# Optimization experiments

Hardware: AMD Instinct MI355X
Metric: run time of the kernel (lower is better)

Reference implementation:

```python
import jax, jax.numpy as jnp
import numpy as np

N_NODES = 50000
HEADS1 = 4
NEG_SLOPE = 0.2
EPS = 1e-16


def gat_conv(x, edge_index, W, att_src, att_dst, bias, heads, out_ch, concat):
    # edge_index: [2, E] with self-loops already appended by caller
    src, dst = edge_index[0], edge_index[1]
    N = x.shape[0]
    h = (x @ W).reshape(N, heads, out_ch)                      # [N, H, C]
    a_src = jnp.sum(h * att_src, axis=-1)                      # [N, H]
    a_dst = jnp.sum(h * att_dst, axis=-1)                      # [N, H]
    e = a_src[src] + a_dst[dst]                                # [E, H]
    e = jnp.where(e > 0, e, NEG_SLOPE * e)                     # leaky_relu
    m = jax.ops.segment_max(e, dst, num_segments=N)            # [N, H]
    alpha = jnp.exp(e - m[dst])                                # [E, H]
    denom = jax.ops.segment_sum(alpha, dst, num_segments=N)    # [N, H]
    alpha = alpha / (denom[dst] + EPS)                         # [E, H]
    msg = alpha[:, :, None] * h[src]                           # [E, H, C]
    out = jax.ops.segment_sum(msg, dst, num_segments=N)        # [N, H, C]
    if concat:
        out = out.reshape(N, heads * out_ch)
    else:
        out = out.mean(axis=1)
    return out + bias, alpha


def setup_inputs() -> dict:
    key = jax.random.key(0)
    ks = jax.random.split(key, 12)
    N, F, H, heads, C, E = N_NODES, 256, 64, HEADS1, 40, 800000
    g = 0.1
    return {
        "x": jax.random.normal(ks[0], (N, F), dtype=jnp.float32),
        "edge_index": jax.random.randint(ks[1], (2, E), 0, N, dtype=jnp.int32),
        "W1": jax.random.normal(ks[2], (F, heads * H), dtype=jnp.float32) * g,
        "att_src1": jax.random.normal(ks[3], (heads, H), dtype=jnp.float32) * g,
        "att_dst1": jax.random.normal(ks[4], (heads, H), dtype=jnp.float32) * g,
        "b1": jnp.zeros((heads * H,), dtype=jnp.float32),
        "W2": jax.random.normal(ks[5], (heads * H, C), dtype=jnp.float32) * g,
        "att_src2": jax.random.normal(ks[6], (1, C), dtype=jnp.float32) * g,
        "att_dst2": jax.random.normal(ks[7], (1, C), dtype=jnp.float32) * g,
        "b2": jnp.zeros((C,), dtype=jnp.float32),
    }


def reference(x, edge_index, W1, att_src1, att_dst1, b1, W2, att_src2, att_dst2, b2):
    N = x.shape[0]
    # add self-loops (PyG GATConv default)
    loops = jnp.arange(N, dtype=edge_index.dtype)
    ei = jnp.concatenate([edge_index, jnp.stack([loops, loops])], axis=1)
    # dropout is identity in eval mode
    h1, alpha = gat_conv(x, ei, W1, att_src1, att_dst1, b1,
                         HEADS1, W1.shape[1] // HEADS1, concat=True)
    h1 = jax.nn.elu(h1)
    h2, _ = gat_conv(h1, ei, W2, att_src2, att_dst2, b2,
                     1, W2.shape[1], concat=False)
    return jax.nn.log_softmax(h2, axis=1), alpha
```

## Files before the change

kernel.cpp:

```cpp
#include <hip/hip_runtime.h>
#include <math.h>

#define N_NODES 50000
#define HC1 256
#define H1 4
#define C2 40
#define C2P 64
#define E0 800000
#define ET 850000
#define NEG_SLOPE 0.2f
#define EPS_A 1e-16f

typedef __bf16 bf16x8 __attribute__((ext_vector_type(8)));
typedef float f32x4 __attribute__((ext_vector_type(4)));
typedef unsigned short u16x8 __attribute__((ext_vector_type(8)));


__device__ inline unsigned short f2bf(float f) {
    unsigned u = __float_as_uint(f);
    return (unsigned short)((u + 0x7FFFu + ((u >> 16) & 1u)) >> 16);
}
__device__ inline float bf2f(unsigned short h) { return __uint_as_float(((unsigned)h) << 16); }
__device__ inline float bf_lo(unsigned q) { return __uint_as_float(q << 16); }
__device__ inline float bf_hi(unsigned q) { return __uint_as_float(q & 0xFFFF0000u); }


__global__ void fill_int_kernel(int* __restrict__ p, int n, int v) {
    int i = blockIdx.x * blockDim.x + threadIdx.x;
    if (i < n) p[i] = v;
}

__device__ inline int edge_src(const int* __restrict__ ei, int e) {
    return (e < E0) ? ei[e] : (e - E0);
}
__device__ inline int edge_dst(const int* __restrict__ ei, int e) {
    return (e < E0) ? ei[E0 + e] : (e - E0);
}


__global__ void f32_to_bf16_kernel(const float* __restrict__ src,
                                   unsigned short* __restrict__ dst, int n4) {
    int i = blockIdx.x * blockDim.x + threadIdx.x;
    if (i >= n4) return;
    float4 v = ((const float4*)src)[i];
    ushort4 w;
    w.x = f2bf(v.x); w.y = f2bf(v.y); w.z = f2bf(v.z); w.w = f2bf(v.w);
    ((ushort4*)dst)[i] = w;
}

__global__ void w1_transpose_kernel(const float* __restrict__ W1,
                                    unsigned short* __restrict__ Wt) {
    int tid = blockIdx.x * blockDim.x + threadIdx.x;
    if (tid >= 256 * 256) return;
    int n = tid >> 8, k = tid & 255;
    Wt[tid] = f2bf(W1[k * 256 + n]);
}

__global__ void w2_transpose_pad_kernel(const float* __restrict__ W2,
                                        unsigned short* __restrict__ Wt) {
    int tid = blockIdx.x * blockDim.x + threadIdx.x;
    if (tid >= 64 * 256) return;
    int n = tid >> 8, k = tid & 255;
    Wt[tid] = (n < C2) ? f2bf(W2[k * C2 + n]) : (unsigned short)0;
}


__global__ void hist_kernel(const int* __restrict__ ei, int* __restrict__ deg) {
    int e = blockIdx.x * blockDim.x + threadIdx.x;
    if (e >= ET) return;
    atomicAdd(&deg[edge_dst(ei, e)], 1);
}

__global__ __launch_bounds__(256) void scan_block_kernel(const int* __restrict__ deg,
                                                         int* __restrict__ excl,
                                                         int* __restrict__ bsum) {
    __shared__ int tmp[256];
    int t = threadIdx.x;
    int i = blockIdx.x * 256 + t;
    int v = (i < N_NODES) ? deg[i] : 0;
    tmp[t] = v;
    __syncthreads();
#pragma unroll
    for (int o = 1; o < 256; o <<= 1) {
        int x = (t >= o) ? tmp[t - o] : 0;
        __syncthreads();
        tmp[t] += x;
        __syncthreads();
    }
    if (i < N_NODES) excl[i] = tmp[t] - v;
    if (t == 255) bsum[blockIdx.x] = tmp[255];
}

#define NSCAN_B 196

__global__ __launch_bounds__(256) void scan_top_kernel(int* __restrict__ bsum) {
    __shared__ int tmp[256];
    int t = threadIdx.x;
    int v = (t < NSCAN_B) ? bsum[t] : 0;
    tmp[t] = v;
    __syncthreads();
#pragma unroll
    for (int o = 1; o < 256; o <<= 1) {
        int x = (t >= o) ? tmp[t - o] : 0;
        __syncthreads();
        tmp[t] += x;
        __syncthreads();
    }
    if (t < NSCAN_B) bsum[t] = tmp[t] - v;
}

__global__ __launch_bounds__(256) void scan_add_kernel(int* __restrict__ offsets,
                                                       int* __restrict__ cursor,
                                                       const int* __restrict__ bsum) {
    int i = blockIdx.x * 256 + threadIdx.x;
    if (i < N_NODES) {
        int v = offsets[i] + bsum[blockIdx.x];
        offsets[i] = v;
        cursor[i] = v;
    }
    if (i == 0) offsets[N_NODES] = ET;
}

__global__ void scatter_kernel(const int* __restrict__ ei, int* __restrict__ cursor,
                               int2* __restrict__ csr_es) {
    int e = blockIdx.x * blockDim.x + threadIdx.x;
    if (e >= ET) return;
    int d = edge_dst(ei, e);
    int pos = atomicAdd(&cursor[d], 1);
    csr_es[pos] = make_int2(e, edge_src(ei, e));
}


template <int TBM, int TBN, int WROWS, int WCOLS>
__global__ __launch_bounds__(256) void gemm_mfma_kernel(const unsigned short* __restrict__ Abf,
                                                        const unsigned short* __restrict__ Bt,
                                                        unsigned short* __restrict__ Cbf,
                                                        const float* __restrict__ att_s,
                                                        const float* __restrict__ att_d,
                                                        float* __restrict__ a_src_o,
                                                        float* __restrict__ a_dst_o,
                                                        int M, int Nc, int attN, int hstride) {
    static_assert(TBM == WROWS * 64 && TBN == WCOLS * 64, "tile");
    constexpr int LDK = 40;
    __shared__ alignas(16) unsigned short As[TBM * LDK];
    __shared__ alignas(16) unsigned short Bs[TBN * LDK];
    const int t = threadIdx.x;
    const int lane = t & 63;
    const int w = t >> 6;
    const int quad = lane >> 4;
    const int l16 = lane & 15;
    const int wm = (w / WCOLS) * 64;
    const int wn = (w % WCOLS) * 64;
    const int bm = blockIdx.x * TBM;
    const int bn = blockIdx.y * TBN;

    f32x4 acc[4][4] = {};

    for (int k0 = 0; k0 < 256; k0 += 32) {
        __syncthreads();
#pragma unroll
        for (int i = 0; i < TBM / 64; ++i) {
            int idx = t + i * 256;
            int row = idx >> 2, seg = idx & 3;
            u16x8 v = {};
            if (bm + row < M)
                v = *(const u16x8*)(Abf + (size_t)(bm + row) * 256 + k0 + seg * 8);
            *(u16x8*)&As[row * LDK + seg * 8] = v;
        }
#pragma unroll
        for (int i = 0; i < TBN / 64; ++i) {
            int idx = t + i * 256;
            int row = idx >> 2, seg = idx & 3;
            u16x8 v = *(const u16x8*)(Bt + (size_t)(bn + row) * 256 + k0 + seg * 8);
            *(u16x8*)&Bs[row * LDK + seg * 8] = v;
        }
        __syncthreads();

        bf16x8 af[4], bfr[4];
#pragma unroll
        for (int mi = 0; mi < 4; ++mi)
            af[mi] = *(const bf16x8*)&As[(wm + mi * 16 + l16) * LDK + quad * 8];
#pragma unroll
        for (int ni = 0; ni < 4; ++ni)
            bfr[ni] = *(const bf16x8*)&Bs[(wn + ni * 16 + l16) * LDK + quad * 8];
#pragma unroll
        for (int mi = 0; mi < 4; ++mi)
#pragma unroll
            for (int ni = 0; ni < 4; ++ni)
                acc[mi][ni] = __builtin_amdgcn_mfma_f32_16x16x32_bf16(
                    af[mi], bfr[ni], acc[mi][ni], 0, 0, 0);
    }

#pragma unroll
    for (int mi = 0; mi < 4; ++mi)
#pragma unroll
        for (int ni = 0; ni < 4; ++ni)
#pragma unroll
            for (int r = 0; r < 4; ++r) {
                int row = bm + wm + mi * 16 + quad * 4 + r;
                int col = bn + wn + ni * 16 + l16;
                if (row < M)
                    Cbf[(size_t)row * Nc + col] = f2bf(acc[mi][ni][r]);
            }

    float asc[4], adc[4];
#pragma unroll
    for (int ni = 0; ni < 4; ++ni) {
        int col = bn + wn + ni * 16 + l16;
        bool valid = col < attN;
        asc[ni] = valid ? att_s[col] : 0.f;
        adc[ni] = valid ? att_d[col] : 0.f;
    }
    float vs[16], vd[16];
#pragma unroll
    for (int mi = 0; mi < 4; ++mi)
#pragma unroll
        for (int r = 0; r < 4; ++r) {
            float s = 0.f, dd = 0.f;
#pragma unroll
            for (int ni = 0; ni < 4; ++ni) {
                s += acc[mi][ni][r] * asc[ni];
                dd += acc[mi][ni][r] * adc[ni];
            }
            vs[mi * 4 + r] = s;
            vd[mi * 4 + r] = dd;
        }
#pragma unroll
    for (int k = 0; k < 4; ++k) {
        const int o = 1 << k;
        const int b = (l16 >> k) & 1;
#pragma unroll
        for (int j = 0; j < (8 >> k); ++j) {
            float lo = vs[2 * j], hi = vs[2 * j + 1];
            float keep = b ? hi : lo, send = b ? lo : hi;
            vs[j] = keep + __shfl_xor(send, o);
            lo = vd[2 * j]; hi = vd[2 * j + 1];
            keep = b ? hi : lo; send = b ? lo : hi;
            vd[j] = keep + __shfl_xor(send, o);
        }
    }
    {
        int mi = l16 >> 2, r = l16 & 3;
        int row = bm + wm + mi * 16 + quad * 4 + r;
        int head = (bn + wn) >> 6;
        if (row < M) {
            a_src_o[(size_t)row * hstride + head] = vs[0];
            a_dst_o[(size_t)row * hstride + head] = vd[0];
        }
    }
}


#define DCAP 512
__global__ __launch_bounds__(256) void l1_fused_kernel(const int* __restrict__ off,
                                                       const int2* __restrict__ csr_es,
                                                       const float* __restrict__ a_src,
                                                       const float* __restrict__ a_dst,
                                                       const unsigned* __restrict__ h1bf,
                                                       const float* __restrict__ b1,
                                                       float* __restrict__ alpha_out,
                                                       unsigned* __restrict__ out1bf) {
    __shared__ int   s_src[DCAP];
    __shared__ int   s_eid[DCAP];
    __shared__ float s_al[H1][DCAP];
    __shared__ float s_stat[H1][2];
    __shared__ float s_comb[2][128][2];
    int d = blockIdx.x;
    int t = threadIdx.x;
    int hd = t >> 6, lane = t & 63;
    int beg = off[d], end = off[d + 1];
    int deg = end - beg;
    float ad = a_dst[d * H1 + hd];

    float elc[8];
    float mx = -INFINITY;
    int c = 0;
    for (int idx = beg + lane; idx < end; idx += 64, ++c) {
        int2 es = csr_es[idx];
        int j = idx - beg;
        if (hd == 0 && j < DCAP) { s_src[j] = es.y; s_eid[j] = es.x; }
        float el = a_src[es.y * H1 + hd] + ad;
        el = el > 0.f ? el : NEG_SLOPE * el;
        if (c < 8) elc[c] = el;
        mx = fmaxf(mx, el);
    }
#pragma unroll
    for (int o = 32; o; o >>= 1) mx = fmaxf(mx, __shfl_xor(mx, o));

    float sum = 0.f;
    c = 0;
    for (int idx = beg + lane; idx < end; idx += 64, ++c) {
        float el;
        if (c < 8) el = elc[c];
        else {
            int2 es = csr_es[idx];
            el = a_src[es.y * H1 + hd] + ad;
            el = el > 0.f ? el : NEG_SLOPE * el;
        }
        float p = __expf(el - mx);
        int j = idx - beg;
        if (j < DCAP) s_al[hd][j] = p;
        sum += p;
    }
#pragma unroll
    for (int o = 32; o; o >>= 1) sum += __shfl_xor(sum, o);
    float inv = 1.f / (sum + EPS_A);
    if (lane == 0) { s_stat[hd][0] = mx; s_stat[hd][1] = inv; }
    __syncthreads();

    int n = min(deg, DCAP);
    {
        float i0 = s_stat[0][1], i1 = s_stat[1][1], i2 = s_stat[2][1], i3 = s_stat[3][1];
        for (int j = t; j < n; j += 256) {
            float4 a4 = make_float4(s_al[0][j] * i0, s_al[1][j] * i1,
                                    s_al[2][j] * i2, s_al[3][j] * i3);
            *(float4*)&alpha_out[(size_t)s_eid[j] * H1] = a4;
        }
    }
    for (int idx = beg + DCAP + lane; idx < end; idx += 64) {
        int2 es = csr_es[idx];
        float el = a_src[es.y * H1 + hd] + ad;
        el = el > 0.f ? el : NEG_SLOPE * el;
        alpha_out[(size_t)es.x * H1 + hd] = __expf(el - mx) * inv;
    }

    int tt = t & 127, eo = t >> 7, head = tt >> 5;
    float acc0 = 0.f, acc1 = 0.f;
    int j = eo;
    for (; j + 6 < n; j += 8) {
        int s0 = s_src[j], s1 = s_src[j + 2], s2 = s_src[j + 4], s3 = s_src[j + 6];
        float a0 = s_al[head][j], a1 = s_al[head][j + 2];
        float a2 = s_al[head][j + 4], a3 = s_al[head][j + 6];
        unsigned q0 = h1bf[(size_t)s0 * 128 + tt];
        unsigned q1 = h1bf[(size_t)s1 * 128 + tt];
        unsigned q2 = h1bf[(size_t)s2 * 128 + tt];
        unsigned q3 = h1bf[(size_t)s3 * 128 + tt];
        acc0 += a0 * bf_lo(q0) + a1 * bf_lo(q1) + a2 * bf_lo(q2) + a3 * bf_lo(q3);
        acc1 += a0 * bf_hi(q0) + a1 * bf_hi(q1) + a2 * bf_hi(q2) + a3 * bf_hi(q3);
    }
    for (; j < n; j += 2) {
        unsigned q = h1bf[(size_t)s_src[j] * 128 + tt];
        float a = s_al[head][j];
        acc0 += a * bf_lo(q);
        acc1 += a * bf_hi(q);
    }
    for (int jj = DCAP + eo; jj < deg; jj += 2) {
        int2 es = csr_es[beg + jj];
        float el = a_src[es.y * H1 + head] + a_dst[d * H1 + head];
        el = el > 0.f ? el : NEG_SLOPE * el;
        float p = __expf(el - s_stat[head][0]);
        unsigned q = h1bf[(size_t)es.y * 128 + tt];
        acc0 += p * bf_lo(q);
        acc1 += p * bf_hi(q);
    }
    s_comb[eo][tt][0] = acc0;
    s_comb[eo][tt][1] = acc1;
    __syncthreads();
    if (t < 128) {
        float invh = s_stat[t >> 5][1];
        float2 bb = *(const float2*)&b1[2 * t];
        float v0 = (s_comb[0][t][0] + s_comb[1][t][0]) * invh + bb.x;
        float v1 = (s_comb[0][t][1] + s_comb[1][t][1]) * invh + bb.y;
        v0 = v0 > 0.f ? v0 : __expf(v0) - 1.f;
        v1 = v1 > 0.f ? v1 : __expf(v1) - 1.f;
        out1bf[(size_t)d * 128 + t] = ((unsigned)f2bf(v1) << 16) | (unsigned)f2bf(v0);
    }
}


__global__ __launch_bounds__(256) void l2_fused_kernel(const int* __restrict__ off,
                                                       const int2* __restrict__ csr_es,
                                                       const float* __restrict__ a_src,
                                                       const float* __restrict__ a_dst,
                                                       const unsigned* __restrict__ h2bf,
                                                       const float* __restrict__ b2,
                                                       float* __restrict__ out) {
    int t = threadIdx.x;
    int lane = t & 63;
    int d = blockIdx.x * 4 + (t >> 6);
    if (d >= N_NODES) return;
    int beg = off[d], end = off[d + 1];
    int deg = end - beg;
    float ad = a_dst[d];
    int nch = (deg + 63) >> 6;

    float elc[4]; int sc[4];
    float mx = -INFINITY;
    for (int cc = 0; cc < nch; ++cc) {
        int idx = beg + cc * 64 + lane;
        float el = -INFINITY; int s = 0;
        if (idx < end) {
            int2 es = csr_es[idx];
            s = es.y;
            el = a_src[s] + ad;
            el = el > 0.f ? el : NEG_SLOPE * el;
        }
        if (cc < 4) { elc[cc] = el; sc[cc] = s; }
        mx = fmaxf(mx, el);
    }
#pragma unroll
    for (int o = 32; o; o >>= 1) mx = fmaxf(mx, __shfl_xor(mx, o));

    float sum = 0.f;
    for (int cc = 0; cc < nch; ++cc) {
        float p;
        if (cc < 4) {
            p = __expf(elc[cc] - mx);
            elc[cc] = p;
        } else {
            int idx = beg + cc * 64 + lane;
            float el = -INFINITY;
            if (idx < end) {
                int2 es = csr_es[idx];
                el = a_src[es.y] + ad;
                el = el > 0.f ? el : NEG_SLOPE * el;
            }
            p = __expf(el - mx);
        }
        sum += p;
    }
#pragma unroll
    for (int o = 32; o; o >>= 1) sum += __shfl_xor(sum, o);
    float inv = 1.f / (sum + EPS_A);

    int half = lane >> 5, li = lane & 31;
    float acc0 = 0.f, acc1 = 0.f;
    for (int cc = 0; cc < nch; ++cc) {
        int cnt = min(64, deg - cc * 64);
        int my_s; float my_a;
        if (cc < 4) {
            my_s = sc[cc];
            my_a = elc[cc];
        } else {
            int idx = beg + cc * 64 + lane;
            my_s = 0; my_a = 0.f;
            if (idx < end) {
                int2 es = csr_es[idx];
                my_s = es.y;
                float el = a_src[es.y] + ad;
                el = el > 0.f ? el : NEG_SLOPE * el;
                my_a = __expf(el - mx);
            }
        }
        for (int j = 0; j < cnt; j += 2) {
            int jj = j + half;
            int s = __shfl(my_s, jj);
            float a = __shfl(my_a, jj);
            if (jj < cnt) {
                unsigned q = h2bf[(size_t)s * 32 + li];
                acc0 += a * bf_lo(q);
                acc1 += a * bf_hi(q);
            }
        }
    }
    acc0 += __shfl_xor(acc0, 32);
    acc1 += __shfl_xor(acc1, 32);
    acc0 *= inv;
    acc1 *= inv;
    bool act = li < 20;
    float v0 = act ? acc0 + b2[2 * li]     : -INFINITY;
    float v1 = act ? acc1 + b2[2 * li + 1] : -INFINITY;
    float mmx = fmaxf(v0, v1);
#pragma unroll
    for (int o = 16; o; o >>= 1) mmx = fmaxf(mmx, __shfl_xor(mmx, o));
    float ex = act ? __expf(v0 - mmx) + __expf(v1 - mmx) : 0.f;
#pragma unroll
    for (int o = 16; o; o >>= 1) ex += __shfl_xor(ex, o);
    float ls = __logf(ex);
    if (act && half == 0)
        *(float2*)&out[(size_t)d * C2 + 2 * li] = make_float2(v0 - mmx - ls, v1 - mmx - ls);
}


extern "C" void kernel_launch(void* const* d_in, const int* in_sizes, int n_in,
                              void* d_out, int out_size, void* d_ws, size_t ws_size,
                              hipStream_t stream) {
    const float* x   = (const float*)d_in[0];
    const int*   ei  = (const int*)d_in[1];
    const float* W1  = (const float*)d_in[2];
    const float* as1 = (const float*)d_in[3];
    const float* ad1 = (const float*)d_in[4];
    const float* b1  = (const float*)d_in[5];
    const float* W2  = (const float*)d_in[6];
    const float* as2 = (const float*)d_in[7];
    const float* ad2 = (const float*)d_in[8];
    const float* b2  = (const float*)d_in[9];

    float* out   = (float*)d_out;
    float* alpha = out + (size_t)N_NODES * C2;

    unsigned* u32    = (unsigned*)d_ws;
    unsigned* h1bf   = u32;
    unsigned* xbf    = h1bf + 6400000;
    unsigned* h2bf   = xbf + 6400000;
    unsigned* w1t    = h2bf + 1600000;
    unsigned* w2t    = w1t + 32768;
    float* a_src1    = (float*)(w2t + 8192);
    float* a_dst1    = a_src1 + 200000;
    float* a_src2    = a_dst1 + 200000;
    float* a_dst2    = a_src2 + 50000;
    int*   deg       = (int*)(a_dst2 + 50000);
    int*   offs      = deg + 50000;
    int*   cursor    = offs + 50001;
    int*   bsum      = cursor + 50000;
    int2*  csr_es    = (int2*)(bsum + 257);
    unsigned* out1bf = xbf;

    const int TB = 256;
    const int EB = (ET + TB - 1) / TB;

    fill_int_kernel<<<(N_NODES + TB - 1) / TB, TB, 0, stream>>>(deg, N_NODES, 0);
    hist_kernel<<<EB, TB, 0, stream>>>(ei, deg);
    scan_block_kernel<<<NSCAN_B, TB, 0, stream>>>(deg, offs, bsum);
    scan_top_kernel<<<1, TB, 0, stream>>>(bsum);
    scan_add_kernel<<<NSCAN_B, TB, 0, stream>>>(offs, cursor, bsum);
    scatter_kernel<<<EB, TB, 0, stream>>>(ei, cursor, csr_es);

    f32_to_bf16_kernel<<<(3200000 + TB - 1) / TB, TB, 0, stream>>>(
        x, (unsigned short*)xbf, 3200000);
    w1_transpose_kernel<<<(65536 + TB - 1) / TB, TB, 0, stream>>>(W1, (unsigned short*)w1t);
    w2_transpose_pad_kernel<<<(16384 + TB - 1) / TB, TB, 0, stream>>>(W2, (unsigned short*)w2t);

    gemm_mfma_kernel<128, 128, 2, 2><<<dim3((N_NODES + 127) / 128, 2), TB, 0, stream>>>(
        (const unsigned short*)xbf, (const unsigned short*)w1t, (unsigned short*)h1bf,
        as1, ad1, a_src1, a_dst1, N_NODES, HC1, 256, H1);
    l1_fused_kernel<<<N_NODES, TB, 0, stream>>>(offs, csr_es, a_src1, a_dst1,
                                                h1bf, b1, alpha, out1bf);

    gemm_mfma_kernel<256, 64, 4, 1><<<dim3((N_NODES + 255) / 256, 1), TB, 0, stream>>>(
        (const unsigned short*)out1bf, (const unsigned short*)w2t, (unsigned short*)h2bf,
        as2, ad2, a_src2, a_dst2, N_NODES, C2P, C2, 1);
    l2_fused_kernel<<<(N_NODES + 3) / 4, TB, 0, stream>>>(offs, csr_es, a_src2, a_dst2,
                                                          h2bf, b2, out);
}
```

Before: 414.2 us.

## Map one wavefront per node in layer-1 GAT aggregation and merge conversion kernels

The layer-1 fused kernel moves from one 256-thread block per destination node to one 64-lane wavefront per node, four nodes per block. Each lane handles all four heads with float4 loads of a_src, a_dst and alpha, and gathers h1 rows with 64-bit loads. The first 64 edges are staged in shared memory, and longer adjacency lists are walked chunk by chunk with shuffle broadcasts. The three input conversion and transpose kernels become one launch, and the softmax shuffle reductions in both layers stop after covering only the active degree. This targets the idle threads and block overhead that come with low average degree, at the cost of less parallelism on high-degree nodes.

Result: faster. 382.0 us (-7.8%).

```diff
diff --git a/kernel.cpp b/kernel.cpp
--- a/kernel.cpp
+++ b/kernel.cpp
@@ -20,7 +20,6 @@
     unsigned u = __float_as_uint(f);
     return (unsigned short)((u + 0x7FFFu + ((u >> 16) & 1u)) >> 16);
 }
-__device__ inline float bf2f(unsigned short h) { return __uint_as_float(((unsigned)h) << 16); }
 __device__ inline float bf_lo(unsigned q) { return __uint_as_float(q << 16); }
 __device__ inline float bf_hi(unsigned q) { return __uint_as_float(q & 0xFFFF0000u); }
 
@@ -38,30 +37,31 @@
 }
 
 
-__global__ void f32_to_bf16_kernel(const float* __restrict__ src,
-                                   unsigned short* __restrict__ dst, int n4) {
-    int i = blockIdx.x * blockDim.x + threadIdx.x;
-    if (i >= n4) return;
-    float4 v = ((const float4*)src)[i];
-    ushort4 w;
-    w.x = f2bf(v.x); w.y = f2bf(v.y); w.z = f2bf(v.z); w.w = f2bf(v.w);
-    ((ushort4*)dst)[i] = w;
-}
-
-__global__ void w1_transpose_kernel(const float* __restrict__ W1,
-                                    unsigned short* __restrict__ Wt) {
+#define CV_X 3200000
+#define CV_W1 65536
+#define CV_W2 16384
+
+__global__ void convert_all_kernel(const float* __restrict__ x,
+                                   const float* __restrict__ W1,
+                                   const float* __restrict__ W2,
+                                   ushort4* __restrict__ xbf,
+                                   unsigned short* __restrict__ w1t,
+                                   unsigned short* __restrict__ w2t) {
     int tid = blockIdx.x * blockDim.x + threadIdx.x;
-    if (tid >= 256 * 256) return;
-    int n = tid >> 8, k = tid & 255;
-    Wt[tid] = f2bf(W1[k * 256 + n]);
-}
-
-__global__ void w2_transpose_pad_kernel(const float* __restrict__ W2,
-                                        unsigned short* __restrict__ Wt) {
-    int tid = blockIdx.x * blockDim.x + threadIdx.x;
-    if (tid >= 64 * 256) return;
-    int n = tid >> 8, k = tid & 255;
-    Wt[tid] = (n < C2) ? f2bf(W2[k * C2 + n]) : (unsigned short)0;
+    if (tid < CV_X) {
+        float4 v = ((const float4*)x)[tid];
+        ushort4 w;
+        w.x = f2bf(v.x); w.y = f2bf(v.y); w.z = f2bf(v.z); w.w = f2bf(v.w);
+        xbf[tid] = w;
+    } else if (tid < CV_X + CV_W1) {
+        int i = tid - CV_X;
+        int n = i >> 8, k = i & 255;
+        w1t[i] = f2bf(W1[k * 256 + n]);
+    } else if (tid < CV_X + CV_W1 + CV_W2) {
+        int i = tid - CV_X - CV_W1;
+        int n = i >> 8, k = i & 255;
+        w2t[i] = (n < C2) ? f2bf(W2[k * C2 + n]) : (unsigned short)0;
+    }
 }
 
 
@@ -251,120 +251,164 @@
 }
 
 
-#define DCAP 512
 __global__ __launch_bounds__(256) void l1_fused_kernel(const int* __restrict__ off,
                                                        const int2* __restrict__ csr_es,
-                                                       const float* __restrict__ a_src,
-                                                       const float* __restrict__ a_dst,
+                                                       const float4* __restrict__ a_src4,
+                                                       const float4* __restrict__ a_dst4,
                                                        const unsigned* __restrict__ h1bf,
                                                        const float* __restrict__ b1,
-                                                       float* __restrict__ alpha_out,
+                                                       float4* __restrict__ alpha_out4,
                                                        unsigned* __restrict__ out1bf) {
-    __shared__ int   s_src[DCAP];
-    __shared__ int   s_eid[DCAP];
-    __shared__ float s_al[H1][DCAP];
-    __shared__ float s_stat[H1][2];
-    __shared__ float s_comb[2][128][2];
-    int d = blockIdx.x;
+    __shared__ int    s_w[4][64];
+    __shared__ float4 a_w[4][64];
     int t = threadIdx.x;
-    int hd = t >> 6, lane = t & 63;
+    int w = t >> 6, lane = t & 63;
+    int d = blockIdx.x * 4 + w;
     int beg = off[d], end = off[d + 1];
     int deg = end - beg;
-    float ad = a_dst[d * H1 + hd];
-
-    float elc[8];
-    float mx = -INFINITY;
-    int c = 0;
-    for (int idx = beg + lane; idx < end; idx += 64, ++c) {
-        int2 es = csr_es[idx];
-        int j = idx - beg;
-        if (hd == 0 && j < DCAP) { s_src[j] = es.y; s_eid[j] = es.x; }
-        float el = a_src[es.y * H1 + hd] + ad;
-        el = el > 0.f ? el : NEG_SLOPE * el;
-        if (c < 8) elc[c] = el;
-        mx = fmaxf(mx, el);
-    }
-#pragma unroll
-    for (int o = 32; o; o >>= 1) mx = fmaxf(mx, __shfl_xor(mx, o));
-
-    float sum = 0.f;
-    c = 0;
-    for (int idx = beg + lane; idx < end; idx += 64, ++c) {
-        float el;
-        if (c < 8) el = elc[c];
-        else {
+    int nch = (deg + 63) >> 6;
+    int cnt0 = min(deg, 64);
+    bool act0 = lane < cnt0;
+    float4 ad4 = a_dst4[d];
+
+    int2  es0 = make_int2(0, 0);
+    float4 l0 = make_float4(-INFINITY, -INFINITY, -INFINITY, -INFINITY);
+    float4 mx = l0;
+    for (int cc = 0; cc < nch; ++cc) {
+        int idx = beg + cc * 64 + lane;
+        float4 l = make_float4(-INFINITY, -INFINITY, -INFINITY, -INFINITY);
+        int2 es = make_int2(0, 0);
+        if (idx < end) {
+            es = csr_es[idx];
+            float4 as4 = a_src4[es.y];
+            l.x = as4.x + ad4.x; l.x = l.x > 0.f ? l.x : NEG_SLOPE * l.x;
+            l.y = as4.y + ad4.y; l.y = l.y > 0.f ? l.y : NEG_SLOPE * l.y;
+            l.z = as4.z + ad4.z; l.z = l.z > 0.f ? l.z : NEG_SLOPE * l.z;
+            l.w = as4.w + ad4.w; l.w = l.w > 0.f ? l.w : NEG_SLOPE * l.w;
+        }
+        if (cc == 0) { es0 = es; l0 = l; }
+        mx.x = fmaxf(mx.x, l.x); mx.y = fmaxf(mx.y, l.y);
+        mx.z = fmaxf(mx.z, l.z); mx.w = fmaxf(mx.w, l.w);
+    }
+    int rdeg = cnt0;
+    for (int o = 1; o < rdeg; o <<= 1) {
+        mx.x = fmaxf(mx.x, __shfl_xor(mx.x, o));
+        mx.y = fmaxf(mx.y, __shfl_xor(mx.y, o));
+        mx.z = fmaxf(mx.z, __shfl_xor(mx.z, o));
+        mx.w = fmaxf(mx.w, __shfl_xor(mx.w, o));
+    }
+    mx.x = __shfl(mx.x, 0); mx.y = __shfl(mx.y, 0);
+    mx.z = __shfl(mx.z, 0); mx.w = __shfl(mx.w, 0);
+
+    float4 p0 = make_float4(0.f, 0.f, 0.f, 0.f);
+    if (act0) {
+        p0.x = __expf(l0.x - mx.x); p0.y = __expf(l0.y - mx.y);
+        p0.z = __expf(l0.z - mx.z); p0.w = __expf(l0.w - mx.w);
+    }
+    float4 sum = p0;
+    for (int cc = 1; cc < nch; ++cc) {
+        int idx = beg + cc * 64 + lane;
+        if (idx < end) {
             int2 es = csr_es[idx];
-            el = a_src[es.y * H1 + hd] + ad;
-            el = el > 0.f ? el : NEG_SLOPE * el;
-        }
-        float p = __expf(el - mx);
-        int j = idx - beg;
-        if (j < DCAP) s_al[hd][j] = p;
-        sum += p;
-    }
-#pragma unroll
-    for (int o = 32; o; o >>= 1) sum += __shfl_xor(sum, o);
-    float inv = 1.f / (sum + EPS_A);
-    if (lane == 0) { s_stat[hd][0] = mx; s_stat[hd][1] = inv; }
+            float4 as4 = a_src4[es.y];
+            float4 l;
+            l.x = as4.x + ad4.x; l.x = l.x > 0.f ? l.x : NEG_SLOPE * l.x;
+            l.y = as4.y + ad4.y; l.y = l.y > 0.f ? l.y : NEG_SLOPE * l.y;
+            l.z = as4.z + ad4.z; l.z = l.z > 0.f ? l.z : NEG_SLOPE * l.z;
+            l.w = as4.w + ad4.w; l.w = l.w > 0.f ? l.w : NEG_SLOPE * l.w;
+            sum.x += __expf(l.x - mx.x); sum.y += __expf(l.y - mx.y);
+            sum.z += __expf(l.z - mx.z); sum.w += __expf(l.w - mx.w);
+        }
+    }
+    for (int o = 1; o < rdeg; o <<= 1) {
+        sum.x += __shfl_xor(sum.x, o);
+        sum.y += __shfl_xor(sum.y, o);
+        sum.z += __shfl_xor(sum.z, o);
+        sum.w += __shfl_xor(sum.w, o);
+    }
+    sum.x = __shfl(sum.x, 0); sum.y = __shfl(sum.y, 0);
+    sum.z = __shfl(sum.z, 0); sum.w = __shfl(sum.w, 0);
+    float4 inv;
+    inv.x = 1.f / (sum.x + EPS_A); inv.y = 1.f / (sum.y + EPS_A);
+    inv.z = 1.f / (sum.z + EPS_A); inv.w = 1.f / (sum.w + EPS_A);
+
+    float4 al0;
+    al0.x = p0.x * inv.x; al0.y = p0.y * inv.y;
+    al0.z = p0.z * inv.z; al0.w = p0.w * inv.w;
+    if (act0) {
+        alpha_out4[es0.x] = al0;
+        s_w[w][lane] = es0.y;
+        a_w[w][lane] = al0;
+    }
     __syncthreads();
 
-    int n = min(deg, DCAP);
-    {
-        float i0 = s_stat[0][1], i1 = s_stat[1][1], i2 = s_stat[2][1], i3 = s_stat[3][1];
-        for (int j = t; j < n; j += 256) {
-            float4 a4 = make_float4(s_al[0][j] * i0, s_al[1][j] * i1,
-                                    s_al[2][j] * i2, s_al[3][j] * i3);
-            *(float4*)&alpha_out[(size_t)s_eid[j] * H1] = a4;
-        }
-    }
-    for (int idx = beg + DCAP + lane; idx < end; idx += 64) {
-        int2 es = csr_es[idx];
-        float el = a_src[es.y * H1 + hd] + ad;
-        el = el > 0.f ? el : NEG_SLOPE * el;
-        alpha_out[(size_t)es.x * H1 + hd] = __expf(el - mx) * inv;
-    }
-
-    int tt = t & 127, eo = t >> 7, head = tt >> 5;
-    float acc0 = 0.f, acc1 = 0.f;
-    int j = eo;
-    for (; j + 6 < n; j += 8) {
-        int s0 = s_src[j], s1 = s_src[j + 2], s2 = s_src[j + 4], s3 = s_src[j + 6];
-        float a0 = s_al[head][j], a1 = s_al[head][j + 2];
-        float a2 = s_al[head][j + 4], a3 = s_al[head][j + 6];
-        unsigned q0 = h1bf[(size_t)s0 * 128 + tt];
-        unsigned q1 = h1bf[(size_t)s1 * 128 + tt];
-        unsigned q2 = h1bf[(size_t)s2 * 128 + tt];
-        unsigned q3 = h1bf[(size_t)s3 * 128 + tt];
-        acc0 += a0 * bf_lo(q0) + a1 * bf_lo(q1) + a2 * bf_lo(q2) + a3 * bf_lo(q3);
-        acc1 += a0 * bf_hi(q0) + a1 * bf_hi(q1) + a2 * bf_hi(q2) + a3 * bf_hi(q3);
-    }
-    for (; j < n; j += 2) {
-        unsigned q = h1bf[(size_t)s_src[j] * 128 + tt];
-        float a = s_al[head][j];
-        acc0 += a * bf_lo(q);
-        acc1 += a * bf_hi(q);
-    }
-    for (int jj = DCAP + eo; jj < deg; jj += 2) {
-        int2 es = csr_es[beg + jj];
-        float el = a_src[es.y * H1 + head] + a_dst[d * H1 + head];
-        el = el > 0.f ? el : NEG_SLOPE * el;
-        float p = __expf(el - s_stat[head][0]);
-        unsigned q = h1bf[(size_t)es.y * 128 + tt];
-        acc0 += p * bf_lo(q);
-        acc1 += p * bf_hi(q);
-    }
-    s_comb[eo][tt][0] = acc0;
-    s_comb[eo][tt][1] = acc1;
-    __syncthreads();
-    if (t < 128) {
-        float invh = s_stat[t >> 5][1];
-        float2 bb = *(const float2*)&b1[2 * t];
-        float v0 = (s_comb[0][t][0] + s_comb[1][t][0]) * invh + bb.x;
-        float v1 = (s_comb[0][t][1] + s_comb[1][t][1]) * invh + bb.y;
-        v0 = v0 > 0.f ? v0 : __expf(v0) - 1.f;
-        v1 = v1 > 0.f ? v1 : __expf(v1) - 1.f;
-        out1bf[(size_t)d * 128 + t] = ((unsigned)f2bf(v1) << 16) | (unsigned)f2bf(v0);
-    }
+    int head = lane >> 4;
+    int base2 = 2 * lane;
+    const float* aw = (const float*)&a_w[w][0];
+    float4 acc = make_float4(0.f, 0.f, 0.f, 0.f);
+    int j = 0;
+    for (; j + 4 <= cnt0; j += 4) {
+        int s0 = s_w[w][j], s1 = s_w[w][j + 1], s2 = s_w[w][j + 2], s3 = s_w[w][j + 3];
+        float A0 = aw[4 * j + head], A1 = aw[4 * j + 4 + head];
+        float A2 = aw[4 * j + 8 + head], A3 = aw[4 * j + 12 + head];
+        uint2 q0 = *(const uint2*)&h1bf[(size_t)s0 * 128 + base2];
+        uint2 q1 = *(const uint2*)&h1bf[(size_t)s1 * 128 + base2];
+        uint2 q2 = *(const uint2*)&h1bf[(size_t)s2 * 128 + base2];
+        uint2 q3 = *(const uint2*)&h1bf[(size_t)s3 * 128 + base2];
+        acc.x += A0 * bf_lo(q0.x) + A1 * bf_lo(q1.x) + A2 * bf_lo(q2.x) + A3 * bf_lo(q3.x);
+        acc.y += A0 * bf_hi(q0.x) + A1 * bf_hi(q1.x) + A2 * bf_hi(q2.x) + A3 * bf_hi(q3.x);
+        acc.z += A0 * bf_lo(q0.y) + A1 * bf_lo(q1.y) + A2 * bf_lo(q2.y) + A3 * bf_lo(q3.y);
+        acc.w += A0 * bf_hi(q0.y) + A1 * bf_hi(q1.y) + A2 * bf_hi(q2.y) + A3 * bf_hi(q3.y);
+    }
+    for (; j < cnt0; ++j) {
+        int s = s_w[w][j];
+        float A = aw[4 * j + head];
+        uint2 q = *(const uint2*)&h1bf[(size_t)s * 128 + base2];
+        acc.x += A * bf_lo(q.x); acc.y += A * bf_hi(q.x);
+        acc.z += A * bf_lo(q.y); acc.w += A * bf_hi(q.y);
+    }
+
+    for (int cc = 1; cc < nch; ++cc) {
+        int idx = beg + cc * 64 + lane;
+        int ms = 0;
+        float4 ma = make_float4(0.f, 0.f, 0.f, 0.f);
+        if (idx < end) {
+            int2 es = csr_es[idx];
+            ms = es.y;
+            float4 as4 = a_src4[es.y];
+            float4 l;
+            l.x = as4.x + ad4.x; l.x = l.x > 0.f ? l.x : NEG_SLOPE * l.x;
+            l.y = as4.y + ad4.y; l.y = l.y > 0.f ? l.y : NEG_SLOPE * l.y;
+            l.z = as4.z + ad4.z; l.z = l.z > 0.f ? l.z : NEG_SLOPE * l.z;
+            l.w = as4.w + ad4.w; l.w = l.w > 0.f ? l.w : NEG_SLOPE * l.w;
+            ma.x = __expf(l.x - mx.x) * inv.x;
+            ma.y = __expf(l.y - mx.y) * inv.y;
+            ma.z = __expf(l.z - mx.z) * inv.z;
+            ma.w = __expf(l.w - mx.w) * inv.w;
+            alpha_out4[es.x] = ma;
+        }
+        int cnt = min(64, deg - cc * 64);
+        for (int jj = 0; jj < cnt; ++jj) {
+            int s = __shfl(ms, jj);
+            float h0 = __shfl(ma.x, jj), h1 = __shfl(ma.y, jj);
+            float h2 = __shfl(ma.z, jj), h3 = __shfl(ma.w, jj);
+            float A = (head & 2) ? ((head & 1) ? h3 : h2) : ((head & 1) ? h1 : h0);
+            uint2 q = *(const uint2*)&h1bf[(size_t)s * 128 + base2];
+            acc.x += A * bf_lo(q.x); acc.y += A * bf_hi(q.x);
+            acc.z += A * bf_lo(q.y); acc.w += A * bf_hi(q.y);
+        }
+    }
+
+    float4 bb = *(const float4*)&b1[4 * lane];
+    float v0 = acc.x + bb.x, v1 = acc.y + bb.y, v2 = acc.z + bb.z, v3 = acc.w + bb.w;
+    v0 = v0 > 0.f ? v0 : __expf(v0) - 1.f;
+    v1 = v1 > 0.f ? v1 : __expf(v1) - 1.f;
+    v2 = v2 > 0.f ? v2 : __expf(v2) - 1.f;
+    v3 = v3 > 0.f ? v3 : __expf(v3) - 1.f;
+    uint2 qo;
+    qo.x = ((unsigned)f2bf(v1) << 16) | (unsigned)f2bf(v0);
+    qo.y = ((unsigned)f2bf(v3) << 16) | (unsigned)f2bf(v2);
+    *(uint2*)&out1bf[(size_t)d * 128 + base2] = qo;
 }
 
 
@@ -398,29 +442,27 @@
         if (cc < 4) { elc[cc] = el; sc[cc] = s; }
         mx = fmaxf(mx, el);
     }
-#pragma unroll
-    for (int o = 32; o; o >>= 1) mx = fmaxf(mx, __shfl_xor(mx, o));
+    int rdeg = min(deg, 64);
+    for (int o = 1; o < rdeg; o <<= 1) mx = fmaxf(mx, __shfl_xor(mx, o));
+    mx = __shfl(mx, 0);
 
     float sum = 0.f;
     for (int cc = 0; cc < nch; ++cc) {
-        float p;
+        int idx = beg + cc * 64 + lane;
+        float p = 0.f;
         if (cc < 4) {
-            p = __expf(elc[cc] - mx);
+            p = (idx < end) ? __expf(elc[cc] - mx) : 0.f;
             elc[cc] = p;
-        } else {
-            int idx = beg + cc * 64 + lane;
-            float el = -INFINITY;
-            if (idx < end) {
-                int2 es = csr_es[idx];
-                el = a_src[es.y] + ad;
-                el = el > 0.f ? el : NEG_SLOPE * el;
-            }
+        } else if (idx < end) {
+            int2 es = csr_es[idx];
+            float el = a_src[es.y] + ad;
+            el = el > 0.f ? el : NEG_SLOPE * el;
             p = __expf(el - mx);
         }
         sum += p;
     }
-#pragma unroll
-    for (int o = 32; o; o >>= 1) sum += __shfl_xor(sum, o);
+    for (int o = 1; o < rdeg; o <<= 1) sum += __shfl_xor(sum, o);
+    sum = __shfl(sum, 0);
     float inv = 1.f / (sum + EPS_A);
 
     int half = lane >> 5, li = lane & 31;
@@ -516,16 +558,16 @@
     scan_add_kernel<<<NSCAN_B, TB, 0, stream>>>(offs, cursor, bsum);
     scatter_kernel<<<EB, TB, 0, stream>>>(ei, cursor, csr_es);
 
-    f32_to_bf16_kernel<<<(3200000 + TB - 1) / TB, TB, 0, stream>>>(
-        x, (unsigned short*)xbf, 3200000);
-    w1_transpose_kernel<<<(65536 + TB - 1) / TB, TB, 0, stream>>>(W1, (unsigned short*)w1t);
-    w2_transpose_pad_kernel<<<(16384 + TB - 1) / TB, TB, 0, stream>>>(W2, (unsigned short*)w2t);
+    convert_all_kernel<<<(CV_X + CV_W1 + CV_W2 + TB - 1) / TB, TB, 0, stream>>>(
+        x, W1, W2, (ushort4*)xbf, (unsigned short*)w1t, (unsigned short*)w2t);
 
     gemm_mfma_kernel<128, 128, 2, 2><<<dim3((N_NODES + 127) / 128, 2), TB, 0, stream>>>(
         (const unsigned short*)xbf, (const unsigned short*)w1t, (unsigned short*)h1bf,
         as1, ad1, a_src1, a_dst1, N_NODES, HC1, 256, H1);
-    l1_fused_kernel<<<N_NODES, TB, 0, stream>>>(offs, csr_es, a_src1, a_dst1,
-                                                h1bf, b1, alpha, out1bf);
+    l1_fused_kernel<<<N_NODES / 4, TB, 0, stream>>>(offs, csr_es,
+                                                    (const float4*)a_src1,
+                                                    (const float4*)a_dst1,
+                                                    h1bf, b1, (float4*)alpha, out1bf);
 
     gemm_mfma_kernel<256, 64, 4, 1><<<dim3((N_NODES + 255) / 256, 1), TB, 0, stream>>>(
         (const unsigned short*)out1bf, (const unsigned short*)w2t, (unsigned short*)h2bf,
```
